# Optimization experiments

Measured on AMD Instinct MI355X. Metric: run time of the kernel, lower is better.

The kernel has to match this reference:

```python
import jax, jax.numpy as jnp
import numpy as np
import math

B, M, DM = 4, 4096, 1024
H, HD = 16, 64            # head_dim = hidden_dim // num_heads
SEG, DIL = 128, 2         # segment_size, dilation_rate
BLOCK_M = 64              # kernel query-block size (min(64, M))
SCALE = HD ** -0.5


def _hilbert_map(seq_len):
    # Faithful port of create_hilbert_mapping_fixed (boustrophedon scan).
    if seq_len <= 64:
        return np.arange(seq_len, dtype=np.int32)
    g = int(math.ceil(math.sqrt(seq_len)))
    mp = np.zeros(seq_len, dtype=np.int64)
    idx = 0
    for row in range(g):
        cols = range(g) if row % 2 == 0 else range(g - 1, -1, -1)
        for col in cols:
            if idx < seq_len:
                lp = row * g + col
                if lp < seq_len:
                    mp[lp] = idx
                    idx += 1
    for i in range(seq_len):
        if i >= idx:
            mp[i] = i
    return mp.astype(np.int32)


def setup_inputs() -> dict:
    key = jax.random.key(0)
    k1, k2, k3 = jax.random.split(key, 3)
    x = jax.random.normal(k1, (B, M, DM), jnp.float32)
    Wqkv = jax.random.normal(k2, (3 * DM, DM), jnp.float32) * 0.02
    Wout = jax.random.normal(k3, (DM, DM), jnp.float32) * 0.02
    hmap = jnp.asarray(_hilbert_map(M))
    return {"x": x, "Wqkv": Wqkv, "Wout": Wout, "hmap": hmap}


def _hilbert_attention(x, Wqkv, Wout, hmap):
    Bn, Mn, _ = x.shape
    qkv = x @ Wqkv.T                                   # [B,M,3*DM]
    qkv = qkv.reshape(Bn, Mn, 3, H, HD).transpose(2, 0, 3, 1, 4)
    q, k, v = qkv[0], qkv[1], qkv[2]                   # [B,H,M,HD]

    S = Mn // SEG           # number of segments
    T = SEG // DIL          # keys per segment (dilated offsets 0, DIL, 2*DIL, ...)
    NB = SEG // BLOCK_M     # query blocks per segment

    # Queries gathered through Hilbert map, pre-scaled (as in kernel).
    qh = q[:, :, hmap, :] * SCALE                      # [B,H,M,HD]

    # Dilated key positions per segment, gathered through Hilbert map.
    key_pos = (jnp.arange(S)[:, None] * SEG + jnp.arange(T)[None, :] * DIL).reshape(-1)
    kh = k[:, :, hmap[key_pos], :].reshape(Bn, H, S, T, HD)
    vh = v[:, :, hmap[key_pos], :].reshape(Bn, H, S, T, HD)

    # Scores per (query-block within segment, key): [B,H,S,NB,BLOCK_M,T]
    qs = qh.reshape(Bn, H, S, NB, BLOCK_M, HD)
    scores = jnp.einsum('bhsnqd,bhstd->bhsnqt', qs, kh)

    # Kernel quirk (faithful): per-KEY max taken over the 64-query block,
    # exp accumulated without rescaling -> NOT a true softmax.
    c = jnp.max(scores, axis=4, keepdims=True)         # max over query block
    w = jnp.exp(scores - c)
    num = jnp.einsum('bhsnqt,bhstd->bhsnqd', w, vh)
    den = 1e-10 + jnp.sum(w, axis=-1, keepdims=True)
    out = (num / den).reshape(Bn, H, Mn, HD)

    # Stored at linear (non-Hilbert) positions, then merged heads + out proj.
    out = out.transpose(0, 2, 1, 3).reshape(Bn, Mn, H * HD)
    return out @ Wout.T


def reference(x, Wqkv, Wout, hmap):
    return _hilbert_attention(x, Wqkv, Wout, hmap)
```

## Files before the change

### kernel.cpp

```cpp
#include <hip/hip_runtime.h>
#include <hip/hip_bf16.h>

#define BB 4
#define MM 4096
#define DM 1024
#define NH 16
#define HDIM 64
#define SEGSZ 128
#define NSEG 32
#define ROWS (BB*MM)
#define QKVC (3*DM)
#define KVROWS (BB*MM/2)
#define KVLD 2048
#define NX4  (ROWS*DM/4)
#define NW14 (QKVC*DM/4)
#define NW24 (DM*DM/4)

typedef __attribute__((ext_vector_type(8))) short bf16x8;
typedef __attribute__((ext_vector_type(4))) float f32x4;

__device__ inline unsigned short f2bf(float f) {
  __hip_bfloat16 h = __float2bfloat16(f);
  return *reinterpret_cast<unsigned short*>(&h);
}

__device__ __forceinline__ void gld16(const ushort* g, ushort* l) {
  __builtin_amdgcn_global_load_lds(
      (const __attribute__((address_space(1))) unsigned int*)g,
      (__attribute__((address_space(3))) unsigned int*)l,
      16, 0, 0);
}

__global__ __launch_bounds__(256) void cvt_all(const float4* __restrict__ x,
                                               const float4* __restrict__ w1,
                                               const float4* __restrict__ w2,
                                               ushort4* __restrict__ xo,
                                               ushort4* __restrict__ w1o,
                                               ushort4* __restrict__ w2o) {
  int i = blockIdx.x * 256 + threadIdx.x;
  const float4* src; ushort4* dst; int off;
  if (i < NX4)              { src = x;  dst = xo;  off = i; }
  else if (i < NX4 + NW14)  { src = w1; dst = w1o; off = i - NX4; }
  else                      { src = w2; dst = w2o; off = i - NX4 - NW14; }
  float4 v = src[off];
  ushort4 o;
  o.x = f2bf(v.x); o.y = f2bf(v.y); o.z = f2bf(v.z); o.w = f2bf(v.w);
  dst[off] = o;
}

#define STAGE_A(T, KH, DB) do {                                              \
    gld16(pA0 + (T) * 64 + (KH) * 32,                                        \
          sAB + ((DB) * 2 + (KH)) * 8192 + wave * 512);                      \
    gld16(pA1 + (T) * 64 + (KH) * 32,                                        \
          sAB + ((DB) * 2 + (KH)) * 8192 + 4096 + wave * 512);               \
  } while (0)
#define STAGE_B(T, KH, DB) do {                                              \
    gld16(pB0 + (T) * 64 + (KH) * 32,                                        \
          sAB + 32768 + ((DB) * 2 + (KH)) * 8192 + wave * 512);              \
    gld16(pB1 + (T) * 64 + (KH) * 32,                                        \
          sAB + 32768 + ((DB) * 2 + (KH)) * 8192 + 4096 + wave * 512);       \
  } while (0)
#define VM6 asm volatile("s_waitcnt vmcnt(6)" ::: "memory")
#define VM8 asm volatile("s_waitcnt vmcnt(8)" ::: "memory")
#define VM0 asm volatile("s_waitcnt vmcnt(0)" ::: "memory")
#define NOPS ((void)0)

#define PH_TAIL(CH)                                                          \
    __builtin_amdgcn_s_barrier();                                            \
    __builtin_amdgcn_s_setprio(1);                                           \
    _Pragma("unroll")                                                        \
    for (int mf = 0; mf < 8; ++mf)                                           \
      _Pragma("unroll")                                                      \
      for (int nf = 0; nf < 2; ++nf)                                         \
        acc[mf][(CH) * 2 + nf] = __builtin_amdgcn_mfma_f32_16x16x32_bf16(    \
            af[mf], bfv[nf], acc[mf][(CH) * 2 + nf], 0, 0, 0);               \
    __builtin_amdgcn_s_setprio(0);                                           \
    __builtin_amdgcn_s_barrier();

#define PH_F_B(AB, BB_, STAGE, VMA) do {                                     \
    const ushort* Ab = (AB); const ushort* Bb = (BB_);                       \
    _Pragma("unroll")                                                        \
    for (int mf = 0; mf < 8; ++mf) {                                         \
      int r = wm * 128 + mf * 16 + m16;                                      \
      af[mf] = *(const bf16x8*)(Ab + r * 32 + ((quad ^ ((r >> 1) & 3)) << 3)); \
    }                                                                        \
    _Pragma("unroll")                                                        \
    for (int nf = 0; nf < 2; ++nf) {                                         \
      int r = wn * 64 + nf * 16 + m16;                                       \
      bfv[nf] = *(const bf16x8*)(Bb + r * 32 + ((quad ^ ((r >> 1) & 3)) << 3)); \
    }                                                                        \
    STAGE; VMA;                                                              \
    PH_TAIL(0)                                                               \
  } while (0)

#define PH_L_B(BB_, STAGE, VMA) do {                                         \
    const ushort* Bb = (BB_);                                                \
    _Pragma("unroll")                                                        \
    for (int nf = 0; nf < 2; ++nf) {                                         \
      int r = wn * 64 + 32 + nf * 16 + m16;                                  \
      bfv[nf] = *(const bf16x8*)(Bb + r * 32 + ((quad ^ ((r >> 1) & 3)) << 3)); \
    }                                                                        \
    STAGE; VMA;                                                              \
    PH_TAIL(1)                                                               \
  } while (0)

#define PH_F(TB, KH, STAGE, VMA) \
    PH_F_B(sAB + ((TB) * 2 + (KH)) * 8192, sAB + 32768 + ((TB) * 2 + (KH)) * 8192, STAGE, VMA)
#define PH_L(TB, KH, STAGE, VMA) \
    PH_L_B(sAB + 32768 + ((TB) * 2 + (KH)) * 8192, STAGE, VMA)

#define KLOOP_1024                                                           \
  STAGE_A(0, 0, 0); STAGE_B(0, 0, 0);                                        \
  STAGE_A(0, 1, 0); STAGE_B(0, 1, 0);                                        \
  STAGE_A(1, 0, 1); STAGE_B(1, 0, 1);                                        \
  VM8;                                                                       \
  __builtin_amdgcn_s_barrier();                                              \
  _Pragma("unroll 1")                                                        \
  for (int i = 0; i < 7; ++i) {                                              \
    const int t1 = 2 * i + 1, t2 = 2 * i + 2, t3 = 2 * i + 3;                \
    PH_F(0, 0, STAGE_A(t1, 1, 1), NOPS);                                     \
    PH_L(0, 0, STAGE_B(t1, 1, 1), VM6);                                      \
    PH_F(0, 1, STAGE_A(t2, 0, 0), NOPS);                                     \
    PH_L(0, 1, STAGE_B(t2, 0, 0), VM6);                                      \
    PH_F(1, 0, STAGE_A(t2, 1, 0), NOPS);                                     \
    PH_L(1, 0, STAGE_B(t2, 1, 0), VM6);                                      \
    PH_F(1, 1, STAGE_A(t3, 0, 1), NOPS);                                     \
    PH_L(1, 1, STAGE_B(t3, 0, 1), VM6);                                      \
  }                                                                          \
  PH_F(0, 0, STAGE_A(15, 1, 1), NOPS);                                       \
  PH_L(0, 0, STAGE_B(15, 1, 1), VM0);                                        \
  _Pragma("unroll 1")                                                        \
  for (int u = 1; u < 4; ++u) {                                              \
    const ushort* AbU = sAB + u * 8192;                                      \
    const ushort* BbU = sAB + 32768 + u * 8192;                              \
    PH_F_B(AbU, BbU, NOPS, NOPS);                                            \
    PH_L_B(BbU, NOPS, NOPS);                                                 \
  }

__global__ __launch_bounds__(512) void gemm_qkv(const ushort* __restrict__ xbf,
                                                const ushort* __restrict__ wqkv,
                                                ushort* __restrict__ qhb,
                                                ushort* __restrict__ kvb,
                                                const int* __restrict__ hmap) {
  __shared__ __align__(16) ushort sAB[65536];
  __shared__ int sRow[256];

  const int blk = blockIdx.x;
  const int tid = threadIdx.x;
  const int lane = tid & 63;
  const int wave = tid >> 6;
  const int m16 = lane & 15;
  const int quad = lane >> 4;
  const int wm = wave >> 2;
  const int wn = wave & 3;

  const int j0 = blk & 255;
  const int swz = (j0 & 7) * 32 + (j0 >> 3);

  const ushort* Bmat; ushort* C; int row0, col0, N;
  if (blk < 256) {
    row0 = (swz >> 2) * 256; col0 = (swz & 3) * 256;
    Bmat = wqkv; C = qhb; N = DM;
  } else {
    row0 = (swz >> 3) * 256; col0 = (swz & 7) * 256;
    Bmat = wqkv + (size_t)DM * DM; C = kvb; N = KVLD;
  }

  if (tid < 256) {
    int m = row0 + tid, xrow;
    if (blk < 256) {
      int b = m >> 12, p = m & 4095;
      xrow = (b << 12) + hmap[p];
    } else {
      int b = m >> 11, idx = m & 2047;
      int ss = idx >> 6, tt = idx & 63;
      xrow = (b << 12) + hmap[ss * SEGSZ + 2 * tt];
    }
    sRow[tid] = xrow;
  }
  __syncthreads();

  const int f0 = wave * 64 + lane, f1 = 512 + f0;
  const int r0 = f0 >> 2, c0 = (f0 & 3) ^ ((f0 >> 3) & 3);
  const int r1 = f1 >> 2, c1 = (f1 & 3) ^ ((f1 >> 3) & 3);
  const ushort* pA0 = xbf + (size_t)sRow[r0] * DM + c0 * 8;
  const ushort* pA1 = xbf + (size_t)sRow[r1] * DM + c1 * 8;
  const ushort* pB0 = Bmat + (size_t)(col0 + r0) * DM + c0 * 8;
  const ushort* pB1 = Bmat + (size_t)(col0 + r1) * DM + c1 * 8;

  f32x4 acc[8][4] = {};
  bf16x8 af[8], bfv[2];

  KLOOP_1024

#pragma unroll
  for (int mf = 0; mf < 8; ++mf)
#pragma unroll
    for (int rr = 0; rr < 4; ++rr) {
      int row = row0 + wm * 128 + mf * 16 + quad * 4 + rr;
#pragma unroll
      for (int nf = 0; nf < 4; ++nf)
        C[(size_t)row * N + col0 + wn * 64 + nf * 16 + m16] = f2bf(acc[mf][nf][rr]);
    }
}

__global__ __launch_bounds__(512) void gemm_out(const ushort* __restrict__ A,
                                                const ushort* __restrict__ Bmat,
                                                float* __restrict__ C) {
  __shared__ __align__(16) ushort sAB[65536];

  const int tid = threadIdx.x;
  const int lane = tid & 63;
  const int wave = tid >> 6;
  const int m16 = lane & 15;
  const int quad = lane >> 4;
  const int wm = wave >> 2;
  const int wn = wave & 3;

  const int j0 = blockIdx.x;
  const int swz = (j0 & 7) * 32 + (j0 >> 3);
  const int row0 = (swz >> 2) * 256;
  const int col0 = (swz & 3) * 256;

  const int f0 = wave * 64 + lane, f1 = 512 + f0;
  const int r0 = f0 >> 2, c0 = (f0 & 3) ^ ((f0 >> 3) & 3);
  const int r1 = f1 >> 2, c1 = (f1 & 3) ^ ((f1 >> 3) & 3);
  const ushort* pA0 = A + (size_t)(row0 + r0) * DM + c0 * 8;
  const ushort* pA1 = A + (size_t)(row0 + r1) * DM + c1 * 8;
  const ushort* pB0 = Bmat + (size_t)(col0 + r0) * DM + c0 * 8;
  const ushort* pB1 = Bmat + (size_t)(col0 + r1) * DM + c1 * 8;

  f32x4 acc[8][4] = {};
  bf16x8 af[8], bfv[2];

  KLOOP_1024

#pragma unroll
  for (int mf = 0; mf < 8; ++mf)
#pragma unroll
    for (int rr = 0; rr < 4; ++rr) {
      int row = row0 + wm * 128 + mf * 16 + quad * 4 + rr;
#pragma unroll
      for (int nf = 0; nf < 4; ++nf)
        C[(size_t)row * DM + col0 + wn * 64 + nf * 16 + m16] = acc[mf][nf][rr];
    }
}

#undef KLOOP_1024
#undef PH_F
#undef PH_L
#undef PH_F_B
#undef PH_L_B
#undef PH_TAIL
#undef STAGE_A
#undef STAGE_B
#undef VM6
#undef VM8
#undef VM0
#undef NOPS

__global__ __launch_bounds__(256) void attn_kernel(const ushort* __restrict__ qh,
                                                   const ushort* __restrict__ kv,
                                                   ushort* __restrict__ out) {
  __shared__ __align__(16) ushort sQW[128 * 72];
  __shared__ __align__(16) ushort sK[64 * 72];
  __shared__ __align__(16) ushort sVT[64 * 72];
  __shared__ float sCmaxW[4 * 64];
  __shared__ float sDen[128];

  const int bid = blockIdx.x;
  const int s  = bid & 31;
  const int h  = (bid >> 5) & 15;
  const int b  = bid >> 9;
  const int tid = threadIdx.x;
  const int lane = tid & 63;
  const int wave = tid >> 6;
  const int m16 = lane & 15;
  const int quad = lane >> 4;
  const int qb = wave * 32;
  const int hb = wave >> 1;

  {
    const int qr = tid >> 1;
    const int qc = (tid & 1) * 32;
    const ushort* qrow = qh + (size_t)(b * MM + s * SEGSZ + qr) * DM + h * HDIM + qc;
    *(uint4*)(sQW + qr * 72 + qc)      = ((const uint4*)qrow)[0];
    *(uint4*)(sQW + qr * 72 + qc + 8)  = ((const uint4*)qrow)[1];
    *(uint4*)(sQW + qr * 72 + qc + 16) = ((const uint4*)qrow)[2];
    *(uint4*)(sQW + qr * 72 + qc + 24) = ((const uint4*)qrow)[3];

    const int r = tid >> 2;
    const int c = (tid & 3) * 16;
    const ushort* krow = kv + (size_t)(b * (MM/2) + s * 64 + r) * KVLD + h * HDIM + c;
    const ushort* vrow = krow + DM;
    *(uint4*)(sK + r * 72 + c)     = ((const uint4*)krow)[0];
    *(uint4*)(sK + r * 72 + c + 8) = ((const uint4*)krow)[1];
    ushort vv[16];
    *(uint4*)(vv)     = ((const uint4*)vrow)[0];
    *(uint4*)(vv + 8) = ((const uint4*)vrow)[1];
#pragma unroll
    for (int u = 0; u < 16; ++u) sVT[(c + u) * 72 + r] = vv[u];
  }
  __syncthreads();

  f32x4 sc[2][4];
  {
    bf16x8 aq[2][2], bk[4][2];
#pragma unroll
    for (int ks = 0; ks < 2; ++ks) {
#pragma unroll
      for (int ib = 0; ib < 2; ++ib)
        aq[ib][ks] = *(const bf16x8*)(sQW + (qb + ib * 16 + m16) * 72 + ks * 32 + quad * 8);
#pragma unroll
      for (int j = 0; j < 4; ++j)
        bk[j][ks] = *(const bf16x8*)(sK + (j * 16 + m16) * 72 + ks * 32 + quad * 8);
    }
#pragma unroll
    for (int ib = 0; ib < 2; ++ib)
#pragma unroll
      for (int j = 0; j < 4; ++j) {
        f32x4 a = {};
        a = __builtin_amdgcn_mfma_f32_16x16x32_bf16(aq[ib][0], bk[j][0], a, 0, 0, 0);
        a = __builtin_amdgcn_mfma_f32_16x16x32_bf16(aq[ib][1], bk[j][1], a, 0, 0, 0);
        sc[ib][j] = a * 0.125f;
      }
  }

#pragma unroll
  for (int j = 0; j < 4; ++j) {
    float m = -1e30f;
#pragma unroll
    for (int ib = 0; ib < 2; ++ib)
#pragma unroll
      for (int r = 0; r < 4; ++r) m = fmaxf(m, sc[ib][j][r]);
    m = fmaxf(m, __shfl_xor(m, 16));
    m = fmaxf(m, __shfl_xor(m, 32));
    if (quad == 0) sCmaxW[wave * 64 + j * 16 + m16] = m;
  }
  __syncthreads();

  {
    float part[2][4] = {};
#pragma unroll
    for (int j = 0; j < 4; ++j) {
      const int col = j * 16 + m16;
      float c0 = fmaxf(sCmaxW[hb * 128 + col], sCmaxW[hb * 128 + 64 + col]);
#pragma unroll
      for (int ib = 0; ib < 2; ++ib)
#pragma unroll
        for (int r = 0; r < 4; ++r) {
          float ww = __expf(sc[ib][j][r] - c0);
          sc[ib][j][r] = ww;
          part[ib][r] += ww;
        }
    }
#pragma unroll
    for (int ib = 0; ib < 2; ++ib)
#pragma unroll
      for (int r = 0; r < 4; ++r) {
        float p = part[ib][r];
        p += __shfl_xor(p, 1); p += __shfl_xor(p, 2);
        p += __shfl_xor(p, 4); p += __shfl_xor(p, 8);
        if (m16 == 0) sDen[qb + ib * 16 + quad * 4 + r] = p;
      }
#pragma unroll
    for (int ib = 0; ib < 2; ++ib)
#pragma unroll
      for (int j = 0; j < 4; ++j)
#pragma unroll
        for (int r = 0; r < 4; ++r)
          sQW[(qb + ib * 16 + quad * 4 + r) * 72 + j * 16 + m16] = f2bf(sc[ib][j][r]);
  }
  __syncthreads();

  f32x4 o[2][4] = {};
  {
    bf16x8 aw[2][2], bv[4][2];
#pragma unroll
    for (int ks = 0; ks < 2; ++ks) {
#pragma unroll
      for (int ib = 0; ib < 2; ++ib)
        aw[ib][ks] = *(const bf16x8*)(sQW + (qb + ib * 16 + m16) * 72 + ks * 32 + quad * 8);
#pragma unroll
      for (int j = 0; j < 4; ++j)
        bv[j][ks] = *(const bf16x8*)(sVT + (j * 16 + m16) * 72 + ks * 32 + quad * 8);
    }
#pragma unroll
    for (int ib = 0; ib < 2; ++ib)
#pragma unroll
      for (int j = 0; j < 4; ++j) {
        o[ib][j] = __builtin_amdgcn_mfma_f32_16x16x32_bf16(aw[ib][0], bv[j][0], o[ib][j], 0, 0, 0);
        o[ib][j] = __builtin_amdgcn_mfma_f32_16x16x32_bf16(aw[ib][1], bv[j][1], o[ib][j], 0, 0, 0);
      }
  }

#pragma unroll
  for (int ib = 0; ib < 2; ++ib)
#pragma unroll
    for (int r = 0; r < 4; ++r) {
      const int lrow = qb + ib * 16 + quad * 4 + r;
      float rd = 1.0f / (1e-10f + sDen[lrow]);
      ushort* op = out + (size_t)(b * MM + s * SEGSZ + lrow) * DM + h * HDIM + m16;
#pragma unroll
      for (int j = 0; j < 4; ++j)
        op[j * 16] = f2bf(o[ib][j][r] * rd);
    }
}

extern "C" void kernel_launch(void* const* d_in, const int* in_sizes, int n_in,
                              void* d_out, int out_size, void* d_ws, size_t ws_size,
                              hipStream_t stream) {
  const float* x    = (const float*)d_in[0];
  const float* wqkv = (const float*)d_in[1];
  const float* wout = (const float*)d_in[2];
  const int*   hmap = (const int*)d_in[3];
  float* outp = (float*)d_out;

  ushort* xbf    = (ushort*)d_ws;
  ushort* wqkvbf = xbf + (size_t)ROWS * DM;
  ushort* woutbf = wqkvbf + (size_t)QKVC * DM;
  ushort* qhb    = woutbf + (size_t)DM * DM;
  ushort* kvb    = qhb + (size_t)ROWS * DM;
  ushort* attn   = kvb + (size_t)KVROWS * KVLD;

  cvt_all<<<(NX4 + NW14 + NW24 + 255) / 256, 256, 0, stream>>>(
      (const float4*)x, (const float4*)wqkv, (const float4*)wout,
      (ushort4*)xbf, (ushort4*)wqkvbf, (ushort4*)woutbf);

  gemm_qkv<<<512, 512, 0, stream>>>(xbf, wqkvbf, qhb, kvb, hmap);

  attn_kernel<<<BB * NH * NSEG, 256, 0, stream>>>(qhb, kvb, attn);

  gemm_out<<<256, 512, 0, stream>>>(attn, woutbf, outp);
}
```

Before: 264.0 us.

## Merge GEMM half-phases into single phase per K-half with shallower prefetch

The shared K-loop macro used by the QKV and output GEMMs changes from two half-phases per LDS K-slice to one phase. Each wave now loads all four B fragments and issues all 32 MFMAs after a single barrier, instead of two groups of 16 separated by two barriers each. A and B staging are merged into one macro, and the prefetch distance drops from three K-slices to two, waiting with vmcnt(4). The standalone drain loop becomes four unrolled phases at the end. The aim is to halve the number of barriers and issue larger MFMA bursts. In exchange it holds more fragment registers and keeps less global-load latency in flight.

Measured after the change: 252.2 us. -4.5%, faster.

```diff
diff --git a/kernel.cpp b/kernel.cpp
--- a/kernel.cpp
+++ b/kernel.cpp
@@ -48,94 +48,62 @@
   dst[off] = o;
 }
 
-#define STAGE_A(T, KH, DB) do {                                              \
+#define STAGE_AB(T, KH, DB) do {                                             \
     gld16(pA0 + (T) * 64 + (KH) * 32,                                        \
           sAB + ((DB) * 2 + (KH)) * 8192 + wave * 512);                      \
     gld16(pA1 + (T) * 64 + (KH) * 32,                                        \
           sAB + ((DB) * 2 + (KH)) * 8192 + 4096 + wave * 512);               \
-  } while (0)
-#define STAGE_B(T, KH, DB) do {                                              \
     gld16(pB0 + (T) * 64 + (KH) * 32,                                        \
           sAB + 32768 + ((DB) * 2 + (KH)) * 8192 + wave * 512);              \
     gld16(pB1 + (T) * 64 + (KH) * 32,                                        \
           sAB + 32768 + ((DB) * 2 + (KH)) * 8192 + 4096 + wave * 512);       \
   } while (0)
-#define VM6 asm volatile("s_waitcnt vmcnt(6)" ::: "memory")
-#define VM8 asm volatile("s_waitcnt vmcnt(8)" ::: "memory")
+#define VM4 asm volatile("s_waitcnt vmcnt(4)" ::: "memory")
 #define VM0 asm volatile("s_waitcnt vmcnt(0)" ::: "memory")
 #define NOPS ((void)0)
 
-#define PH_TAIL(CH)                                                          \
-    __builtin_amdgcn_s_barrier();                                            \
-    __builtin_amdgcn_s_setprio(1);                                           \
-    _Pragma("unroll")                                                        \
-    for (int mf = 0; mf < 8; ++mf)                                           \
-      _Pragma("unroll")                                                      \
-      for (int nf = 0; nf < 2; ++nf)                                         \
-        acc[mf][(CH) * 2 + nf] = __builtin_amdgcn_mfma_f32_16x16x32_bf16(    \
-            af[mf], bfv[nf], acc[mf][(CH) * 2 + nf], 0, 0, 0);               \
-    __builtin_amdgcn_s_setprio(0);                                           \
-    __builtin_amdgcn_s_barrier();
-
-#define PH_F_B(AB, BB_, STAGE, VMA) do {                                     \
-    const ushort* Ab = (AB); const ushort* Bb = (BB_);                       \
+#define PH_M(TB, KH, STAGE, VMA) do {                                        \
+    const ushort* Ab = sAB + ((TB) * 2 + (KH)) * 8192;                       \
+    const ushort* Bb = sAB + 32768 + ((TB) * 2 + (KH)) * 8192;               \
     _Pragma("unroll")                                                        \
     for (int mf = 0; mf < 8; ++mf) {                                         \
       int r = wm * 128 + mf * 16 + m16;                                      \
       af[mf] = *(const bf16x8*)(Ab + r * 32 + ((quad ^ ((r >> 1) & 3)) << 3)); \
     }                                                                        \
     _Pragma("unroll")                                                        \
-    for (int nf = 0; nf < 2; ++nf) {                                         \
+    for (int nf = 0; nf < 4; ++nf) {                                         \
       int r = wn * 64 + nf * 16 + m16;                                       \
       bfv[nf] = *(const bf16x8*)(Bb + r * 32 + ((quad ^ ((r >> 1) & 3)) << 3)); \
     }                                                                        \
     STAGE; VMA;                                                              \
-    PH_TAIL(0)                                                               \
+    __builtin_amdgcn_s_barrier();                                            \
+    __builtin_amdgcn_s_setprio(1);                                           \
+    _Pragma("unroll")                                                        \
+    for (int mf = 0; mf < 8; ++mf)                                           \
+      _Pragma("unroll")                                                      \
+      for (int nf = 0; nf < 4; ++nf)                                         \
+        acc[mf][nf] = __builtin_amdgcn_mfma_f32_16x16x32_bf16(               \
+            af[mf], bfv[nf], acc[mf][nf], 0, 0, 0);                          \
+    __builtin_amdgcn_s_setprio(0);                                           \
   } while (0)
 
-#define PH_L_B(BB_, STAGE, VMA) do {                                         \
-    const ushort* Bb = (BB_);                                                \
-    _Pragma("unroll")                                                        \
-    for (int nf = 0; nf < 2; ++nf) {                                         \
-      int r = wn * 64 + 32 + nf * 16 + m16;                                  \
-      bfv[nf] = *(const bf16x8*)(Bb + r * 32 + ((quad ^ ((r >> 1) & 3)) << 3)); \
-    }                                                                        \
-    STAGE; VMA;                                                              \
-    PH_TAIL(1)                                                               \
-  } while (0)
-
-#define PH_F(TB, KH, STAGE, VMA) \
-    PH_F_B(sAB + ((TB) * 2 + (KH)) * 8192, sAB + 32768 + ((TB) * 2 + (KH)) * 8192, STAGE, VMA)
-#define PH_L(TB, KH, STAGE, VMA) \
-    PH_L_B(sAB + 32768 + ((TB) * 2 + (KH)) * 8192, STAGE, VMA)
-
 #define KLOOP_1024                                                           \
-  STAGE_A(0, 0, 0); STAGE_B(0, 0, 0);                                        \
-  STAGE_A(0, 1, 0); STAGE_B(0, 1, 0);                                        \
-  STAGE_A(1, 0, 1); STAGE_B(1, 0, 1);                                        \
-  VM8;                                                                       \
+  STAGE_AB(0, 0, 0);                                                         \
+  STAGE_AB(0, 1, 0);                                                         \
+  VM4;                                                                       \
   __builtin_amdgcn_s_barrier();                                              \
   _Pragma("unroll 1")                                                        \
   for (int i = 0; i < 7; ++i) {                                              \
-    const int t1 = 2 * i + 1, t2 = 2 * i + 2, t3 = 2 * i + 3;                \
-    PH_F(0, 0, STAGE_A(t1, 1, 1), NOPS);                                     \
-    PH_L(0, 0, STAGE_B(t1, 1, 1), VM6);                                      \
-    PH_F(0, 1, STAGE_A(t2, 0, 0), NOPS);                                     \
-    PH_L(0, 1, STAGE_B(t2, 0, 0), VM6);                                      \
-    PH_F(1, 0, STAGE_A(t2, 1, 0), NOPS);                                     \
-    PH_L(1, 0, STAGE_B(t2, 1, 0), VM6);                                      \
-    PH_F(1, 1, STAGE_A(t3, 0, 1), NOPS);                                     \
-    PH_L(1, 1, STAGE_B(t3, 0, 1), VM6);                                      \
+    const int t1 = 2 * i + 1, t2 = 2 * i + 2;                                \
+    PH_M(0, 0, STAGE_AB(t1, 0, 1), VM4);                                     \
+    PH_M(0, 1, STAGE_AB(t1, 1, 1), VM4);                                     \
+    PH_M(1, 0, STAGE_AB(t2, 0, 0), VM4);                                     \
+    PH_M(1, 1, STAGE_AB(t2, 1, 0), VM4);                                     \
   }                                                                          \
-  PH_F(0, 0, STAGE_A(15, 1, 1), NOPS);                                       \
-  PH_L(0, 0, STAGE_B(15, 1, 1), VM0);                                        \
-  _Pragma("unroll 1")                                                        \
-  for (int u = 1; u < 4; ++u) {                                              \
-    const ushort* AbU = sAB + u * 8192;                                      \
-    const ushort* BbU = sAB + 32768 + u * 8192;                              \
-    PH_F_B(AbU, BbU, NOPS, NOPS);                                            \
-    PH_L_B(BbU, NOPS, NOPS);                                                 \
-  }
+  PH_M(0, 0, STAGE_AB(15, 0, 1), VM4);                                       \
+  PH_M(0, 1, STAGE_AB(15, 1, 1), VM4);                                       \
+  PH_M(1, 0, NOPS, VM0);                                                     \
+  PH_M(1, 1, NOPS, NOPS);
 
 __global__ __launch_bounds__(512) void gemm_qkv(const ushort* __restrict__ xbf,
                                                 const ushort* __restrict__ wqkv,
@@ -189,7 +157,7 @@
   const ushort* pB1 = Bmat + (size_t)(col0 + r1) * DM + c1 * 8;
 
   f32x4 acc[8][4] = {};
-  bf16x8 af[8], bfv[2];
+  bf16x8 af[8], bfv[4];
 
   KLOOP_1024
 
@@ -231,7 +199,7 @@
   const ushort* pB1 = Bmat + (size_t)(col0 + r1) * DM + c1 * 8;
 
   f32x4 acc[8][4] = {};
-  bf16x8 af[8], bfv[2];
+  bf16x8 af[8], bfv[4];
 
   KLOOP_1024
 
@@ -247,15 +215,9 @@
 }
 
 #undef KLOOP_1024
-#undef PH_F
-#undef PH_L
-#undef PH_F_B
-#undef PH_L_B
-#undef PH_TAIL
-#undef STAGE_A
-#undef STAGE_B
-#undef VM6
-#undef VM8
+#undef PH_M
+#undef STAGE_AB
+#undef VM4
 #undef VM0
 #undef NOPS
 
```
